# Kernel optimization log

Hardware: AMD Instinct MI355X
Metric: run time of the kernel (lower is better)

Reference implementation:

```python
import jax, jax.numpy as jnp
import numpy as np

N = 50000      # nodes
E = 800000     # edges (avg degree 16)
F_IN = 128     # num_node_features
H = 128        # hidden_channels


def setup_inputs() -> dict:
    key = jax.random.key(0)
    ks = jax.random.split(key, 9)
    x = jax.random.normal(ks[0], (N, F_IN), jnp.float32)
    edge_index = jax.random.randint(ks[1], (2, E), 0, N, dtype=jnp.int64)
    s_in = 1.0 / np.sqrt(F_IN)
    s_h = 1.0 / np.sqrt(H)
    return {
        "x": x,
        "edge_index": edge_index,
        "W1": jax.random.normal(ks[2], (F_IN, H), jnp.float32) * s_in,
        "b1": jax.random.normal(ks[3], (H,), jnp.float32) * 0.01,
        "W2": jax.random.normal(ks[4], (H, H), jnp.float32) * s_h,
        "b2": jax.random.normal(ks[5], (H,), jnp.float32) * 0.01,
        "W3": jax.random.normal(ks[6], (H, H), jnp.float32) * s_h,
        "b3": jax.random.normal(ks[7], (H,), jnp.float32) * 0.01,
    }


def gcn_layer(x, src_f, dst_f, dinv, W, b):
    # PyG GCNConv: out = D^-1/2 (A+I) D^-1/2 (x @ W) + b
    h = x @ W                                   # [N, H]
    coef = dinv[src_f] * dinv[dst_f]            # [E+N]
    msg = coef[:, None] * h[src_f]              # gather + scale, [E+N, H]
    agg = jax.ops.segment_sum(msg, dst_f, num_segments=x.shape[0])
    return agg + b


def reference(x, edge_index, W1, b1, W2, b2, W3, b3):
    n = x.shape[0]
    loops = jnp.arange(n, dtype=edge_index.dtype)
    src_f = jnp.concatenate([edge_index[0], loops])  # edges + self loops
    dst_f = jnp.concatenate([edge_index[1], loops])
    # degree with unit edge weights (edge_weight=None)
    deg = jax.ops.segment_sum(jnp.ones(src_f.shape[0], x.dtype), dst_f, num_segments=n)
    dinv = jnp.where(deg > 0, jax.lax.rsqrt(deg), 0.0)
    h = jax.nn.relu(gcn_layer(x, src_f, dst_f, dinv, W1, b1))
    # dropout p=0.1 is identity in eval mode
    h = jax.nn.relu(gcn_layer(h, src_f, dst_f, dinv, W2, b2))
    return gcn_layer(h, src_f, dst_f, dinv, W3, b3)
```

## Files before the change

kernel.cpp:

```cpp
#include <hip/hip_runtime.h>

#define HDIM 128
#define BM 64
#define CAP 64
#define CSH 4

typedef _Float16 half8 __attribute__((ext_vector_type(8)));
typedef _Float16 half2v __attribute__((ext_vector_type(2)));
typedef float f32x4 __attribute__((ext_vector_type(4)));


__global__ void prep_k(const float* __restrict__ W1, const float* __restrict__ W2,
                       const float* __restrict__ W3,
                       _Float16* __restrict__ Wp1, _Float16* __restrict__ Wp2,
                       _Float16* __restrict__ Wp3,
                       int* __restrict__ cntp, int n) {
    int i = blockIdx.x * blockDim.x + threadIdx.x;
    int stride = gridDim.x * blockDim.x;
    for (int j = i; j < (n << CSH); j += stride) cntp[j] = 0;
    for (int j = i; j < HDIM * HDIM; j += stride) {
        int k = j >> 7, col = j & 127;
        size_t p = ((size_t)(k >> 3) * HDIM + col) * 8 + (k & 7);
        Wp1[p] = (_Float16)W1[j];
        Wp2[p] = (_Float16)W2[j];
        Wp3[p] = (_Float16)W3[j];
    }
}


__global__ void fill_k(const int* __restrict__ src, const int* __restrict__ dst,
                       int* __restrict__ cntp, int* __restrict__ slots, int E) {
    int e = blockIdx.x * blockDim.x + threadIdx.x;
    if (e >= E) return;
    int s = src[e], d = dst[e];
    int p = atomicAdd(&cntp[d << CSH], 1);
    if (p < CAP) slots[(size_t)d * CAP + p] = s;
}


template <bool A32>
__global__ __launch_bounds__(256) void gemm_h(const void* __restrict__ Ain,
                                              const _Float16* __restrict__ Wp,
                                              const int* __restrict__ cntp,
                                              _Float16* __restrict__ C, int n) {
    const int lane = threadIdx.x & 63;
    const int wave = threadIdx.x >> 6;
    const int row0 = blockIdx.x * BM + wave * 16;
    const int rlo  = lane & 15;
    const int khi  = lane >> 4;

    f32x4 acc[8] = {};

#pragma unroll
    for (int s = 0; s < 4; ++s) {
        half8 a = {};
        int arow = row0 + rlo;
        if (arow < n) {
            if constexpr (A32) {
                const float* Af = (const float*)Ain;
                const float4* p0 = (const float4*)&Af[(size_t)arow * HDIM + 32 * s + 8 * khi];
                float4 lo = p0[0], hi = p0[1];
                a[0] = (_Float16)lo.x; a[1] = (_Float16)lo.y;
                a[2] = (_Float16)lo.z; a[3] = (_Float16)lo.w;
                a[4] = (_Float16)hi.x; a[5] = (_Float16)hi.y;
                a[6] = (_Float16)hi.z; a[7] = (_Float16)hi.w;
            } else {
                a = *(const half8*)&((const _Float16*)Ain)[(size_t)arow * HDIM + 32 * s + 8 * khi];
            }
        }
        const int kb = 4 * s + khi;
#pragma unroll
        for (int c = 0; c < 8; ++c) {
            half8 b = *(const half8*)&Wp[((size_t)kb * HDIM + 16 * c + rlo) * 8];
            acc[c] = __builtin_amdgcn_mfma_f32_16x16x32_f16(a, b, acc[c], 0, 0, 0);
        }
    }

    float dr[4];
#pragma unroll
    for (int r = 0; r < 4; ++r) {
        int row = row0 + khi * 4 + r;
        dr[r] = (row < n) ? rsqrtf((float)(cntp[row << CSH] + 1)) : 0.f;
    }

#pragma unroll
    for (int c = 0; c < 8; ++c) {
        int col = 16 * c + rlo;
#pragma unroll
        for (int r = 0; r < 4; ++r) {
            int row = row0 + khi * 4 + r;
            if (row < n) C[(size_t)row * HDIM + col] = (_Float16)(dr[r] * acc[c][r]);
        }
    }
}


__global__ __launch_bounds__(256) void agg_h(const _Float16* __restrict__ h,
                                             const int* __restrict__ cntp,
                                             const int* __restrict__ slots,
                                             const float* __restrict__ bias,
                                             _Float16* __restrict__ out16,
                                             float* __restrict__ out32,
                                             int n, int relu) {
    int node = blockIdx.x * 4 + (threadIdx.x >> 6);
    int lane = threadIdx.x & 63;
    if (node >= n) return;

    const half2v* hp = (const half2v*)h;
    int deg = cntp[node << CSH];
    float di = rsqrtf((float)(deg + 1));
    if (deg > CAP) deg = CAP;

    half2v sv = hp[(size_t)node * 64 + lane];
    float ax = (float)sv[0];
    float ay = (float)sv[1];

    const int* el = &slots[(size_t)node * CAP];

    int e = 0;
    for (; e + 8 <= deg; e += 8) {
        int s[8];
#pragma unroll
        for (int u = 0; u < 8; ++u) s[u] = el[e + u];
        half2v v[8];
#pragma unroll
        for (int u = 0; u < 8; ++u) v[u] = hp[(size_t)s[u] * 64 + lane];
#pragma unroll
        for (int u = 0; u < 8; ++u) {
            ax += (float)v[u][0];
            ay += (float)v[u][1];
        }
    }
    for (; e < deg; ++e) {
        half2v v = hp[(size_t)el[e] * 64 + lane];
        ax += (float)v[0];
        ay += (float)v[1];
    }

    float2 b = ((const float2*)bias)[lane];
    ax = di * ax + b.x;
    ay = di * ay + b.y;
    if (relu) { ax = fmaxf(ax, 0.f); ay = fmaxf(ay, 0.f); }

    if (out16) {
        half2v o = { (_Float16)ax, (_Float16)ay };
        ((half2v*)out16)[(size_t)node * 64 + lane] = o;
    } else {
        float2 o; o.x = ax; o.y = ay;
        ((float2*)out32)[(size_t)node * 64 + lane] = o;
    }
}


extern "C" void kernel_launch(void* const* d_in, const int* in_sizes, int n_in,
                              void* d_out, int out_size, void* d_ws, size_t ws_size,
                              hipStream_t stream) {
    const float* x  = (const float*)d_in[0];
    const int*   ei = (const int*)d_in[1];
    const float* W1 = (const float*)d_in[2];
    const float* b1 = (const float*)d_in[3];
    const float* W2 = (const float*)d_in[4];
    const float* b2 = (const float*)d_in[5];
    const float* W3 = (const float*)d_in[6];
    const float* b3 = (const float*)d_in[7];
    float* out = (float*)d_out;

    const int n = in_sizes[0] / HDIM;
    const int E = in_sizes[1] / 2;
    const int* src = ei;
    const int* dst = ei + E;

    char* p = (char*)d_ws;
    auto alloc = [&](size_t bytes) {
        char* r = p;
        p += (bytes + 255) & ~(size_t)255;
        return r;
    };
    int*       cntp  = (int*)  alloc(((size_t)n << CSH) * 4);
    int*       slots = (int*)  alloc((size_t)n * CAP * 4);
    _Float16*  Wp1   = (_Float16*)alloc(HDIM * HDIM * 2);
    _Float16*  Wp2   = (_Float16*)alloc(HDIM * HDIM * 2);
    _Float16*  Wp3   = (_Float16*)alloc(HDIM * HDIM * 2);
    _Float16*  bufA  = (_Float16*)alloc(((size_t)n + 64) * HDIM * 2);
    _Float16*  bufG  = (_Float16*)alloc(((size_t)n + 64) * HDIM * 2);

    prep_k<<<1024, 256, 0, stream>>>(W1, W2, W3, Wp1, Wp2, Wp3, cntp, n);
    fill_k<<<(E + 255) / 256, 256, 0, stream>>>(src, dst, cntp, slots, E);

    const int gb = (n + BM - 1) / BM;
    const int ab = (n + 3) / 4;

    gemm_h<true><<<gb, 256, 0, stream>>>(x, Wp1, cntp, bufG, n);
    agg_h<<<ab, 256, 0, stream>>>(bufG, cntp, slots, b1, bufA, nullptr, n, 1);
    gemm_h<false><<<gb, 256, 0, stream>>>(bufA, Wp2, cntp, bufG, n);
    agg_h<<<ab, 256, 0, stream>>>(bufG, cntp, slots, b2, bufA, nullptr, n, 1);
    gemm_h<false><<<gb, 256, 0, stream>>>(bufA, Wp3, cntp, bufG, n);
    agg_h<<<ab, 256, 0, stream>>>(bufG, cntp, slots, b3, nullptr, out, n, 0);
}
```

Baseline: 291.5 us.

## Fuse edge bucketing into first GEMM and split aggregation across half-waves

```diff
diff --git a/kernel.cpp b/kernel.cpp
--- a/kernel.cpp
+++ b/kernel.cpp
@@ -6,7 +6,7 @@
 #define CSH 4
 
 typedef _Float16 half8 __attribute__((ext_vector_type(8)));
-typedef _Float16 half2v __attribute__((ext_vector_type(2)));
+typedef _Float16 half4 __attribute__((ext_vector_type(4)));
 typedef float f32x4 __attribute__((ext_vector_type(4)));
 
 
@@ -28,18 +28,75 @@
 }
 
 
-__global__ void fill_k(const int* __restrict__ src, const int* __restrict__ dst,
-                       int* __restrict__ cntp, int* __restrict__ slots, int E) {
+__global__ __launch_bounds__(256) void gemmfill_k(const float* __restrict__ A,
+                                                  const _Float16* __restrict__ Wp,
+                                                  _Float16* __restrict__ C,
+                                                  const int* __restrict__ src,
+                                                  const int* __restrict__ dst,
+                                                  int* __restrict__ cntp,
+                                                  int* __restrict__ slots,
+                                                  int n, int E) {
+    const int stride = gridDim.x * blockDim.x;
     int e = blockIdx.x * blockDim.x + threadIdx.x;
-    if (e >= E) return;
-    int s = src[e], d = dst[e];
-    int p = atomicAdd(&cntp[d << CSH], 1);
-    if (p < CAP) slots[(size_t)d * CAP + p] = s;
-}
-
-
-template <bool A32>
-__global__ __launch_bounds__(256) void gemm_h(const void* __restrict__ Ain,
+    for (; e + 3 * stride < E; e += 4 * stride) {
+        int s0 = src[e],              d0 = dst[e];
+        int s1 = src[e + stride],     d1 = dst[e + stride];
+        int s2 = src[e + 2 * stride], d2 = dst[e + 2 * stride];
+        int s3 = src[e + 3 * stride], d3 = dst[e + 3 * stride];
+        int p0 = atomicAdd(&cntp[d0 << CSH], 1);
+        int p1 = atomicAdd(&cntp[d1 << CSH], 1);
+        int p2 = atomicAdd(&cntp[d2 << CSH], 1);
+        int p3 = atomicAdd(&cntp[d3 << CSH], 1);
+        if (p0 < CAP) slots[(size_t)d0 * CAP + p0] = s0;
+        if (p1 < CAP) slots[(size_t)d1 * CAP + p1] = s1;
+        if (p2 < CAP) slots[(size_t)d2 * CAP + p2] = s2;
+        if (p3 < CAP) slots[(size_t)d3 * CAP + p3] = s3;
+    }
+    for (; e < E; e += stride) {
+        int s = src[e], d = dst[e];
+        int p = atomicAdd(&cntp[d << CSH], 1);
+        if (p < CAP) slots[(size_t)d * CAP + p] = s;
+    }
+
+    const int lane = threadIdx.x & 63;
+    const int wave = threadIdx.x >> 6;
+    const int row0 = blockIdx.x * BM + wave * 16;
+    const int rlo  = lane & 15;
+    const int khi  = lane >> 4;
+
+    f32x4 acc[8] = {};
+#pragma unroll
+    for (int s = 0; s < 4; ++s) {
+        half8 a = {};
+        int arow = row0 + rlo;
+        if (arow < n) {
+            const float4* p0 = (const float4*)&A[(size_t)arow * HDIM + 32 * s + 8 * khi];
+            float4 lo = p0[0], hi = p0[1];
+            a[0] = (_Float16)lo.x; a[1] = (_Float16)lo.y;
+            a[2] = (_Float16)lo.z; a[3] = (_Float16)lo.w;
+            a[4] = (_Float16)hi.x; a[5] = (_Float16)hi.y;
+            a[6] = (_Float16)hi.z; a[7] = (_Float16)hi.w;
+        }
+        const int kb = 4 * s + khi;
+#pragma unroll
+        for (int c = 0; c < 8; ++c) {
+            half8 b = *(const half8*)&Wp[((size_t)kb * HDIM + 16 * c + rlo) * 8];
+            acc[c] = __builtin_amdgcn_mfma_f32_16x16x32_f16(a, b, acc[c], 0, 0, 0);
+        }
+    }
+#pragma unroll
+    for (int c = 0; c < 8; ++c) {
+        int col = 16 * c + rlo;
+#pragma unroll
+        for (int r = 0; r < 4; ++r) {
+            int row = row0 + khi * 4 + r;
+            if (row < n) C[(size_t)row * HDIM + col] = (_Float16)acc[c][r];
+        }
+    }
+}
+
+
+__global__ __launch_bounds__(256) void gemm_h(const _Float16* __restrict__ A,
                                               const _Float16* __restrict__ Wp,
                                               const int* __restrict__ cntp,
                                               _Float16* __restrict__ C, int n) {
@@ -50,24 +107,12 @@
     const int khi  = lane >> 4;
 
     f32x4 acc[8] = {};
-
 #pragma unroll
     for (int s = 0; s < 4; ++s) {
         half8 a = {};
         int arow = row0 + rlo;
-        if (arow < n) {
-            if constexpr (A32) {
-                const float* Af = (const float*)Ain;
-                const float4* p0 = (const float4*)&Af[(size_t)arow * HDIM + 32 * s + 8 * khi];
-                float4 lo = p0[0], hi = p0[1];
-                a[0] = (_Float16)lo.x; a[1] = (_Float16)lo.y;
-                a[2] = (_Float16)lo.z; a[3] = (_Float16)lo.w;
-                a[4] = (_Float16)hi.x; a[5] = (_Float16)hi.y;
-                a[6] = (_Float16)hi.z; a[7] = (_Float16)hi.w;
-            } else {
-                a = *(const half8*)&((const _Float16*)Ain)[(size_t)arow * HDIM + 32 * s + 8 * khi];
-            }
-        }
+        if (arow < n)
+            a = *(const half8*)&A[(size_t)arow * HDIM + 32 * s + 8 * khi];
         const int kb = 4 * s + khi;
 #pragma unroll
         for (int c = 0; c < 8; ++c) {
@@ -82,7 +127,6 @@
         int row = row0 + khi * 4 + r;
         dr[r] = (row < n) ? rsqrtf((float)(cntp[row << CSH] + 1)) : 0.f;
     }
-
 #pragma unroll
     for (int c = 0; c < 8; ++c) {
         int col = 16 * c + rlo;
@@ -95,59 +139,93 @@
 }
 
 
+template <bool DINV, bool OUT16>
 __global__ __launch_bounds__(256) void agg_h(const _Float16* __restrict__ h,
                                              const int* __restrict__ cntp,
                                              const int* __restrict__ slots,
                                              const float* __restrict__ bias,
-                                             _Float16* __restrict__ out16,
-                                             float* __restrict__ out32,
+                                             void* __restrict__ outp,
                                              int n, int relu) {
     int node = blockIdx.x * 4 + (threadIdx.x >> 6);
-    int lane = threadIdx.x & 63;
     if (node >= n) return;
-
-    const half2v* hp = (const half2v*)h;
+    const int lane = threadIdx.x & 63;
+    const int sub  = lane >> 5;
+    const int li   = lane & 31;
+
+    const half4* hp = (const half4*)h;
     int deg = cntp[node << CSH];
     float di = rsqrtf((float)(deg + 1));
     if (deg > CAP) deg = CAP;
-
-    half2v sv = hp[(size_t)node * 64 + lane];
-    float ax = (float)sv[0];
-    float ay = (float)sv[1];
-
+    const int items = deg + 1;
     const int* el = &slots[(size_t)node * CAP];
 
-    int e = 0;
-    for (; e + 8 <= deg; e += 8) {
-        int s[8];
-#pragma unroll
-        for (int u = 0; u < 8; ++u) s[u] = el[e + u];
-        half2v v[8];
-#pragma unroll
-        for (int u = 0; u < 8; ++u) v[u] = hp[(size_t)s[u] * 64 + lane];
-#pragma unroll
-        for (int u = 0; u < 8; ++u) {
-            ax += (float)v[u][0];
-            ay += (float)v[u][1];
-        }
-    }
-    for (; e < deg; ++e) {
-        half2v v = hp[(size_t)el[e] * 64 + lane];
-        ax += (float)v[0];
-        ay += (float)v[1];
-    }
-
-    float2 b = ((const float2*)bias)[lane];
-    ax = di * ax + b.x;
-    ay = di * ay + b.y;
-    if (relu) { ax = fmaxf(ax, 0.f); ay = fmaxf(ay, 0.f); }
-
-    if (out16) {
-        half2v o = { (_Float16)ax, (_Float16)ay };
-        ((half2v*)out16)[(size_t)node * 64 + lane] = o;
-    } else {
-        float2 o; o.x = ax; o.y = ay;
-        ((float2*)out32)[(size_t)node * 64 + lane] = o;
+    float ax = 0.f, ay = 0.f, az = 0.f, aw = 0.f;
+
+    int i = 0;
+    for (; i + 8 <= items; i += 8) {
+        int idx[4];
+#pragma unroll
+        for (int u = 0; u < 4; ++u) {
+            int ii = i + 2 * u + sub;
+            idx[u] = (ii == 0) ? node : el[ii - 1];
+        }
+        half4 v[4];
+#pragma unroll
+        for (int u = 0; u < 4; ++u) v[u] = hp[(size_t)idx[u] * 32 + li];
+        float sc[4];
+#pragma unroll
+        for (int u = 0; u < 4; ++u) {
+            if constexpr (DINV) {
+                int ii = i + 2 * u + sub;
+                sc[u] = (ii == 0) ? di : rsqrtf((float)(cntp[idx[u] << CSH] + 1));
+            } else sc[u] = 1.f;
+        }
+#pragma unroll
+        for (int u = 0; u < 4; ++u) {
+            ax += sc[u] * (float)v[u][0];
+            ay += sc[u] * (float)v[u][1];
+            az += sc[u] * (float)v[u][2];
+            aw += sc[u] * (float)v[u][3];
+        }
+    }
+    for (; i < items; i += 2) {
+        int ii = i + sub;
+        bool live = ii < items;
+        int r = (live && ii >= 1) ? el[ii - 1] : node;
+        half4 v = hp[(size_t)r * 32 + li];
+        float sc;
+        if constexpr (DINV)
+            sc = (ii == 0) ? di : rsqrtf((float)(cntp[r << CSH] + 1));
+        else sc = 1.f;
+        if (!live) sc = 0.f;
+        ax += sc * (float)v[0];
+        ay += sc * (float)v[1];
+        az += sc * (float)v[2];
+        aw += sc * (float)v[3];
+    }
+
+    ax += __shfl_xor(ax, 32);
+    ay += __shfl_xor(ay, 32);
+    az += __shfl_xor(az, 32);
+    aw += __shfl_xor(aw, 32);
+
+    float4 b4 = ((const float4*)bias)[li];
+    ax = di * ax + b4.x;
+    ay = di * ay + b4.y;
+    az = di * az + b4.z;
+    aw = di * aw + b4.w;
+    if (relu) {
+        ax = fmaxf(ax, 0.f); ay = fmaxf(ay, 0.f);
+        az = fmaxf(az, 0.f); aw = fmaxf(aw, 0.f);
+    }
+    if (sub == 0) {
+        if constexpr (OUT16) {
+            half4 o = { (_Float16)ax, (_Float16)ay, (_Float16)az, (_Float16)aw };
+            ((half4*)outp)[(size_t)node * 32 + li] = o;
+        } else {
+            float4 o = make_float4(ax, ay, az, aw);
+            ((float4*)outp)[(size_t)node * 32 + li] = o;
+        }
     }
 }
 
@@ -184,16 +262,14 @@
     _Float16*  bufA  = (_Float16*)alloc(((size_t)n + 64) * HDIM * 2);
     _Float16*  bufG  = (_Float16*)alloc(((size_t)n + 64) * HDIM * 2);
 
-    prep_k<<<1024, 256, 0, stream>>>(W1, W2, W3, Wp1, Wp2, Wp3, cntp, n);
-    fill_k<<<(E + 255) / 256, 256, 0, stream>>>(src, dst, cntp, slots, E);
-
     const int gb = (n + BM - 1) / BM;
     const int ab = (n + 3) / 4;
 
-    gemm_h<true><<<gb, 256, 0, stream>>>(x, Wp1, cntp, bufG, n);
-    agg_h<<<ab, 256, 0, stream>>>(bufG, cntp, slots, b1, bufA, nullptr, n, 1);
-    gemm_h<false><<<gb, 256, 0, stream>>>(bufA, Wp2, cntp, bufG, n);
-    agg_h<<<ab, 256, 0, stream>>>(bufG, cntp, slots, b2, bufA, nullptr, n, 1);
-    gemm_h<false><<<gb, 256, 0, stream>>>(bufA, Wp3, cntp, bufG, n);
-    agg_h<<<ab, 256, 0, stream>>>(bufG, cntp, slots, b3, nullptr, out, n, 0);
-}
+    prep_k<<<1024, 256, 0, stream>>>(W1, W2, W3, Wp1, Wp2, Wp3, cntp, n);
+    gemmfill_k<<<gb, 256, 0, stream>>>(x, Wp1, bufG, src, dst, cntp, slots, n, E);
+    agg_h<true, true><<<ab, 256, 0, stream>>>(bufG, cntp, slots, b1, bufA, n, 1);
+    gemm_h<<<gb, 256, 0, stream>>>(bufA, Wp2, cntp, bufG, n);
+    agg_h<false, true><<<ab, 256, 0, stream>>>(bufG, cntp, slots, b2, bufA, n, 1);
+    gemm_h<<<gb, 256, 0, stream>>>(bufA, Wp3, cntp, bufG, n);
+    agg_h<false, false><<<ab, 256, 0, stream>>>(bufG, cntp, slots, b3, out, n, 0);
+}
```

Result: no change. 288.2 us (-1.1%).

## Build adjacency with LDS-partitioned counters and widen aggregation to half4 half-waves

Applied to the files above, without the earlier changes.

```diff
diff --git a/kernel.cpp b/kernel.cpp
--- a/kernel.cpp
+++ b/kernel.cpp
@@ -3,45 +3,74 @@
 #define HDIM 128
 #define BM 64
 #define CAP 64
-#define CSH 4
+#define RMAX 6272
 
 typedef _Float16 half8 __attribute__((ext_vector_type(8)));
-typedef _Float16 half2v __attribute__((ext_vector_type(2)));
+typedef _Float16 half4 __attribute__((ext_vector_type(4)));
 typedef float f32x4 __attribute__((ext_vector_type(4)));
 
 
-__global__ void prep_k(const float* __restrict__ W1, const float* __restrict__ W2,
-                       const float* __restrict__ W3,
-                       _Float16* __restrict__ Wp1, _Float16* __restrict__ Wp2,
-                       _Float16* __restrict__ Wp3,
-                       int* __restrict__ cntp, int n) {
-    int i = blockIdx.x * blockDim.x + threadIdx.x;
-    int stride = gridDim.x * blockDim.x;
-    for (int j = i; j < (n << CSH); j += stride) cntp[j] = 0;
-    for (int j = i; j < HDIM * HDIM; j += stride) {
-        int k = j >> 7, col = j & 127;
-        size_t p = ((size_t)(k >> 3) * HDIM + col) * 8 + (k & 7);
-        Wp1[p] = (_Float16)W1[j];
-        Wp2[p] = (_Float16)W2[j];
-        Wp3[p] = (_Float16)W3[j];
-    }
-}
-
-
-__global__ void fill_k(const int* __restrict__ src, const int* __restrict__ dst,
-                       int* __restrict__ cntp, int* __restrict__ slots, int E) {
-    int e = blockIdx.x * blockDim.x + threadIdx.x;
-    if (e >= E) return;
-    int s = src[e], d = dst[e];
-    int p = atomicAdd(&cntp[d << CSH], 1);
-    if (p < CAP) slots[(size_t)d * CAP + p] = s;
+__global__ __launch_bounds__(512) void fillprep_k(
+        const int* __restrict__ src, const int* __restrict__ dst,
+        int* __restrict__ cnt, int* __restrict__ slots,
+        const float* __restrict__ W1, const float* __restrict__ W2,
+        const float* __restrict__ W3,
+        _Float16* __restrict__ Wp1, _Float16* __restrict__ Wp2,
+        _Float16* __restrict__ Wp3, int n, int E) {
+    __shared__ int lcnt[RMAX];
+    const int lo = blockIdx.x * RMAX;
+    const int hi = (lo + RMAX < n) ? lo + RMAX : n;
+    const int R  = hi - lo;
+
+    {
+        int gid  = blockIdx.x * 512 + threadIdx.x;
+        int gstr = gridDim.x * 512;
+        for (int j = gid; j < HDIM * HDIM; j += gstr) {
+            int k = j >> 7, col = j & 127;
+            size_t p = ((size_t)(k >> 3) * HDIM + col) * 8 + (k & 7);
+            Wp1[p] = (_Float16)W1[j];
+            Wp2[p] = (_Float16)W2[j];
+            Wp3[p] = (_Float16)W3[j];
+        }
+    }
+
+    for (int i = threadIdx.x; i < R; i += 512) lcnt[i] = 0;
+    __syncthreads();
+
+    const int4* d4 = (const int4*)dst;
+    const int4* s4 = (const int4*)src;
+    const int nq = E >> 2;
+
+    auto proc = [&](int d, int s) {
+        if (d >= lo && d < hi) {
+            int p = atomicAdd(&lcnt[d - lo], 1);
+            if (p < CAP) slots[(size_t)d * CAP + p] = s;
+        }
+    };
+
+    int q = threadIdx.x;
+    for (; q + 512 < nq; q += 1024) {
+        int4 da = d4[q], db = d4[q + 512];
+        int4 sa = s4[q], sb = s4[q + 512];
+        proc(da.x, sa.x); proc(da.y, sa.y); proc(da.z, sa.z); proc(da.w, sa.w);
+        proc(db.x, sb.x); proc(db.y, sb.y); proc(db.z, sb.z); proc(db.w, sb.w);
+    }
+    for (; q < nq; q += 512) {
+        int4 da = d4[q], sa = s4[q];
+        proc(da.x, sa.x); proc(da.y, sa.y); proc(da.z, sa.z); proc(da.w, sa.w);
+    }
+    for (int e = (nq << 2) + threadIdx.x; e < E; e += 512)
+        proc(dst[e], src[e]);
+
+    __syncthreads();
+    for (int i = threadIdx.x; i < R; i += 512) cnt[lo + i] = lcnt[i];
 }
 
 
 template <bool A32>
 __global__ __launch_bounds__(256) void gemm_h(const void* __restrict__ Ain,
                                               const _Float16* __restrict__ Wp,
-                                              const int* __restrict__ cntp,
+                                              const int* __restrict__ cnt,
                                               _Float16* __restrict__ C, int n) {
     const int lane = threadIdx.x & 63;
     const int wave = threadIdx.x >> 6;
@@ -50,7 +79,6 @@
     const int khi  = lane >> 4;
 
     f32x4 acc[8] = {};
-
 #pragma unroll
     for (int s = 0; s < 4; ++s) {
         half8 a = {};
@@ -59,11 +87,11 @@
             if constexpr (A32) {
                 const float* Af = (const float*)Ain;
                 const float4* p0 = (const float4*)&Af[(size_t)arow * HDIM + 32 * s + 8 * khi];
-                float4 lo = p0[0], hi = p0[1];
-                a[0] = (_Float16)lo.x; a[1] = (_Float16)lo.y;
-                a[2] = (_Float16)lo.z; a[3] = (_Float16)lo.w;
-                a[4] = (_Float16)hi.x; a[5] = (_Float16)hi.y;
-                a[6] = (_Float16)hi.z; a[7] = (_Float16)hi.w;
+                float4 lov = p0[0], hiv = p0[1];
+                a[0] = (_Float16)lov.x; a[1] = (_Float16)lov.y;
+                a[2] = (_Float16)lov.z; a[3] = (_Float16)lov.w;
+                a[4] = (_Float16)hiv.x; a[5] = (_Float16)hiv.y;
+                a[6] = (_Float16)hiv.z; a[7] = (_Float16)hiv.w;
             } else {
                 a = *(const half8*)&((const _Float16*)Ain)[(size_t)arow * HDIM + 32 * s + 8 * khi];
             }
@@ -80,9 +108,8 @@
 #pragma unroll
     for (int r = 0; r < 4; ++r) {
         int row = row0 + khi * 4 + r;
-        dr[r] = (row < n) ? rsqrtf((float)(cntp[row << CSH] + 1)) : 0.f;
-    }
-
+        dr[r] = (row < n) ? rsqrtf((float)(cnt[row] + 1)) : 0.f;
+    }
 #pragma unroll
     for (int c = 0; c < 8; ++c) {
         int col = 16 * c + rlo;
@@ -95,59 +122,81 @@
 }
 
 
+template <bool OUT16>
 __global__ __launch_bounds__(256) void agg_h(const _Float16* __restrict__ h,
-                                             const int* __restrict__ cntp,
+                                             const int* __restrict__ cnt,
                                              const int* __restrict__ slots,
                                              const float* __restrict__ bias,
-                                             _Float16* __restrict__ out16,
-                                             float* __restrict__ out32,
+                                             void* __restrict__ outp,
                                              int n, int relu) {
     int node = blockIdx.x * 4 + (threadIdx.x >> 6);
-    int lane = threadIdx.x & 63;
     if (node >= n) return;
-
-    const half2v* hp = (const half2v*)h;
-    int deg = cntp[node << CSH];
+    const int lane = threadIdx.x & 63;
+    const int sub  = lane >> 5;
+    const int li   = lane & 31;
+
+    const half4* hp = (const half4*)h;
+    int deg = cnt[node];
     float di = rsqrtf((float)(deg + 1));
     if (deg > CAP) deg = CAP;
-
-    half2v sv = hp[(size_t)node * 64 + lane];
-    float ax = (float)sv[0];
-    float ay = (float)sv[1];
-
+    const int items = deg + 1;
     const int* el = &slots[(size_t)node * CAP];
 
-    int e = 0;
-    for (; e + 8 <= deg; e += 8) {
-        int s[8];
-#pragma unroll
-        for (int u = 0; u < 8; ++u) s[u] = el[e + u];
-        half2v v[8];
-#pragma unroll
-        for (int u = 0; u < 8; ++u) v[u] = hp[(size_t)s[u] * 64 + lane];
-#pragma unroll
-        for (int u = 0; u < 8; ++u) {
+    float ax = 0.f, ay = 0.f, az = 0.f, aw = 0.f;
+
+    int i = 0;
+    for (; i + 8 <= items; i += 8) {
+        int idx[4];
+#pragma unroll
+        for (int u = 0; u < 4; ++u) {
+            int ii = i + 2 * u + sub;
+            idx[u] = (ii == 0) ? node : el[ii - 1];
+        }
+        half4 v[4];
+#pragma unroll
+        for (int u = 0; u < 4; ++u) v[u] = hp[(size_t)idx[u] * 32 + li];
+#pragma unroll
+        for (int u = 0; u < 4; ++u) {
             ax += (float)v[u][0];
             ay += (float)v[u][1];
-        }
-    }
-    for (; e < deg; ++e) {
-        half2v v = hp[(size_t)el[e] * 64 + lane];
-        ax += (float)v[0];
-        ay += (float)v[1];
-    }
-
-    float2 b = ((const float2*)bias)[lane];
-    ax = di * ax + b.x;
-    ay = di * ay + b.y;
-    if (relu) { ax = fmaxf(ax, 0.f); ay = fmaxf(ay, 0.f); }
-
-    if (out16) {
-        half2v o = { (_Float16)ax, (_Float16)ay };
-        ((half2v*)out16)[(size_t)node * 64 + lane] = o;
-    } else {
-        float2 o; o.x = ax; o.y = ay;
-        ((float2*)out32)[(size_t)node * 64 + lane] = o;
+            az += (float)v[u][2];
+            aw += (float)v[u][3];
+        }
+    }
+    for (; i < items; i += 2) {
+        int ii = i + sub;
+        if (ii < items) {
+            int r = (ii == 0) ? node : el[ii - 1];
+            half4 v = hp[(size_t)r * 32 + li];
+            ax += (float)v[0];
+            ay += (float)v[1];
+            az += (float)v[2];
+            aw += (float)v[3];
+        }
+    }
+
+    ax += __shfl_xor(ax, 32);
+    ay += __shfl_xor(ay, 32);
+    az += __shfl_xor(az, 32);
+    aw += __shfl_xor(aw, 32);
+
+    float4 b4 = ((const float4*)bias)[li];
+    ax = di * ax + b4.x;
+    ay = di * ay + b4.y;
+    az = di * az + b4.z;
+    aw = di * aw + b4.w;
+    if (relu) {
+        ax = fmaxf(ax, 0.f); ay = fmaxf(ay, 0.f);
+        az = fmaxf(az, 0.f); aw = fmaxf(aw, 0.f);
+    }
+    if (sub == 0) {
+        if constexpr (OUT16) {
+            half4 o = { (_Float16)ax, (_Float16)ay, (_Float16)az, (_Float16)aw };
+            ((half4*)outp)[(size_t)node * 32 + li] = o;
+        } else {
+            float4 o = make_float4(ax, ay, az, aw);
+            ((float4*)outp)[(size_t)node * 32 + li] = o;
+        }
     }
 }
 
@@ -176,7 +225,7 @@
         p += (bytes + 255) & ~(size_t)255;
         return r;
     };
-    int*       cntp  = (int*)  alloc(((size_t)n << CSH) * 4);
+    int*       cnt   = (int*)  alloc((size_t)n * 4);
     int*       slots = (int*)  alloc((size_t)n * CAP * 4);
     _Float16*  Wp1   = (_Float16*)alloc(HDIM * HDIM * 2);
     _Float16*  Wp2   = (_Float16*)alloc(HDIM * HDIM * 2);
@@ -184,16 +233,16 @@
     _Float16*  bufA  = (_Float16*)alloc(((size_t)n + 64) * HDIM * 2);
     _Float16*  bufG  = (_Float16*)alloc(((size_t)n + 64) * HDIM * 2);
 
-    prep_k<<<1024, 256, 0, stream>>>(W1, W2, W3, Wp1, Wp2, Wp3, cntp, n);
-    fill_k<<<(E + 255) / 256, 256, 0, stream>>>(src, dst, cntp, slots, E);
-
+    const int F  = (n + RMAX - 1) / RMAX;
     const int gb = (n + BM - 1) / BM;
     const int ab = (n + 3) / 4;
 
-    gemm_h<true><<<gb, 256, 0, stream>>>(x, Wp1, cntp, bufG, n);
-    agg_h<<<ab, 256, 0, stream>>>(bufG, cntp, slots, b1, bufA, nullptr, n, 1);
-    gemm_h<false><<<gb, 256, 0, stream>>>(bufA, Wp2, cntp, bufG, n);
-    agg_h<<<ab, 256, 0, stream>>>(bufG, cntp, slots, b2, bufA, nullptr, n, 1);
-    gemm_h<false><<<gb, 256, 0, stream>>>(bufA, Wp3, cntp, bufG, n);
-    agg_h<<<ab, 256, 0, stream>>>(bufG, cntp, slots, b3, nullptr, out, n, 0);
-}
+    fillprep_k<<<F, 512, 0, stream>>>(src, dst, cnt, slots,
+                                      W1, W2, W3, Wp1, Wp2, Wp3, n, E);
+    gemm_h<true><<<gb, 256, 0, stream>>>(x, Wp1, cnt, bufG, n);
+    agg_h<true><<<ab, 256, 0, stream>>>(bufG, cnt, slots, b1, bufA, n, 1);
+    gemm_h<false><<<gb, 256, 0, stream>>>(bufA, Wp2, cnt, bufG, n);
+    agg_h<true><<<ab, 256, 0, stream>>>(bufG, cnt, slots, b2, bufA, n, 1);
+    gemm_h<false><<<gb, 256, 0, stream>>>(bufA, Wp3, cnt, bufG, n);
+    agg_h<false><<<ab, 256, 0, stream>>>(bufG, cnt, slots, b3, out, n, 0);
+}
```

New measurement: 646.1 us. 2.22x slower.
